# Performance work log

Measured on AMD Instinct MI355X. Metric: run time of the kernel, lower is better.

Reference implementation:

```python
import jax, jax.numpy as jnp
import numpy as np

B, T, H = 64, 1024, 256

def _lstm_cell(x, h, c, Wih, Whh, bih, bhh):
    # torch gate order: i, f, g, o
    gates = x @ Wih.T + h @ Whh.T + bih + bhh  # [B, 4H]
    i, f, g, o = jnp.split(gates, 4, axis=-1)
    i = jax.nn.sigmoid(i)
    f = jax.nn.sigmoid(f)
    g = jnp.tanh(g)
    o = jax.nn.sigmoid(o)
    c_new = f * c + i * g
    h_new = o * jnp.tanh(c_new)
    return h_new, c_new


def setup_inputs() -> dict:
    key = jax.random.key(0)
    ks = jax.random.split(key, 11)
    s = 1.0 / np.sqrt(H)
    def u(k, shape):
        return jax.random.uniform(k, shape, jnp.float32, -s, s)
    return {
        "x": jax.random.normal(ks[0], (B, T, 1), jnp.float32),
        "enc_Wih": u(ks[1], (4 * H, 1)),
        "enc_Whh": u(ks[2], (4 * H, H)),
        "enc_bih": u(ks[3], (4 * H,)),
        "enc_bhh": u(ks[4], (4 * H,)),
        "dec_Wih": u(ks[5], (4 * H, 1)),
        "dec_Whh": u(ks[6], (4 * H, H)),
        "dec_bih": u(ks[7], (4 * H,)),
        "dec_bhh": u(ks[8], (4 * H,)),
        "lin_W": u(ks[9], (1, 2 * H)),
        "lin_b": u(ks[10], (1,)),
    }


def reference(x, enc_Wih, enc_Whh, enc_bih, enc_bhh,
              dec_Wih, dec_Whh, dec_bih, dec_bhh, lin_W, lin_b):
    b = x.shape[0]
    h = x.shape[2] * 0  # placeholder, not used
    hidden = enc_Whh.shape[1]

    x_t = jnp.transpose(x, (1, 0, 2))  # [T, B, 1]

    # ---- encoder: single-layer LSTM over time ----
    def enc_step(carry, xt):
        hh, cc = carry
        hh, cc = _lstm_cell(xt, hh, cc, enc_Wih, enc_Whh, enc_bih, enc_bhh)
        return (hh, cc), hh
    h0 = jnp.zeros((b, hidden), x.dtype)
    (h_last, _), enc_seq = jax.lax.scan(enc_step, (h0, h0), x_t)
    encoder_states = jnp.transpose(enc_seq, (1, 0, 2))  # [B, T, H]

    # ---- decoder: LSTMCell + dot attention + linear, per step ----
    def dec_step(carry, xt):
        hx, cx = carry
        hx, cx = _lstm_cell(xt, hx, cx, dec_Wih, dec_Whh, dec_bih, dec_bhh)
        scores = jnp.einsum('bth,bh->bt', encoder_states, hx)  # dot attention
        attn = jax.nn.softmax(scores, axis=1)
        ctx = jnp.einsum('bt,bth->bh', attn, encoder_states)
        updated = jnp.concatenate([ctx, hx], axis=1)  # [B, 2H]
        res = updated @ lin_W.T + lin_b  # [B, 1]
        return (hx, cx), res

    cx0 = jnp.zeros_like(h_last)
    _, outs = jax.lax.scan(dec_step, (h_last, cx0), x_t)  # [T, B, 1]
    return jnp.transpose(outs, (1, 0, 2))  # [B, T, 1]
```

## Files before the change

### kernel.cpp

```cpp
#include <hip/hip_runtime.h>
#include <math.h>

#define HD 256
#define GD 1024
#define TT 1024
#define BB 64
#define NT 512

__device__ __forceinline__ float sig_(float x)  { return 1.f / (1.f + __expf(-x)); }
__device__ __forceinline__ float tanh_(float x) { return 1.f - 2.f / (1.f + __expf(2.f * x)); }

__global__ __launch_bounds__(256) void prep_kernel(
    const float* __restrict__ eW, const float* __restrict__ eb1, const float* __restrict__ eb2,
    const float* __restrict__ dW, const float* __restrict__ db1, const float* __restrict__ db2,
    float* __restrict__ WTe, float* __restrict__ WTd,
    float* __restrict__ be, float* __restrict__ bd,
    unsigned long long* __restrict__ ex_all)
{
    int idx = blockIdx.x * 256 + threadIdx.x;
    if (idx < GD * HD) {
        int j = idx / HD, k = idx % HD;
        WTe[k * GD + j] = eW[idx];
        WTd[k * GD + j] = dW[idx];
    }
    if (idx < GD) {
        be[idx] = eb1[idx] + eb2[idx];
        bd[idx] = db1[idx] + db2[idx];
    }
    if (idx < 2 * BB * 2 * 256) ex_all[idx] = 0ULL;
}

__global__ __launch_bounds__(NT, 2) void lstm_scan_coop(
    const float* __restrict__ x,
    const float* __restrict__ Wih,
    const float* __restrict__ bias,
    const float* __restrict__ WT,
    const float* __restrict__ h_init,
    float* __restrict__ states,
    unsigned long long* __restrict__ ex)
{
    const int b   = blockIdx.x & 63;
    const int q   = blockIdx.x >> 6;
    const int tid = threadIdx.x;
    const int s   = tid & 3;
    const int jj  = tid >> 2;
    const int gate = jj >> 5;
    const int kk0  = (jj & 31) * 2;
    const int r0   = gate * 64 + kk0;
    const int jg0  = gate * 256 + q * 64 + kk0;

    __shared__ float h_rep[4][264];
    __shared__ float act_s[256];
    __shared__ float x_s[TT];

    float4 w0[16], w1[16];
    {
        const float* basek = WT + (size_t)(s * 64) * GD;
        #pragma unroll
        for (int i = 0; i < 16; ++i) {
            const float* p0 = basek + (size_t)(4 * i) * GD + jg0;
            w0[i] = make_float4(p0[0], p0[GD], p0[2 * GD], p0[3 * GD]);
            const float* p1 = p0 + 1;
            w1[i] = make_float4(p1[0], p1[GD], p1[2 * GD], p1[3 * GD]);
        }
    }
    const float wih0 = Wih[jg0], wih1 = Wih[jg0 + 1];
    const float bj0  = bias[jg0], bj1  = bias[jg0 + 1];

    for (int i = tid; i < TT; i += NT) x_s[i] = x[b * TT + i];
    if (tid < 256) {
        float hv = h_init ? h_init[((size_t)b * TT + (TT - 1)) * HD + tid] : 0.f;
        h_rep[tid >> 6][tid & 63] = hv;
    }
    float c = 0.f;
    __syncthreads();

    for (int t = 0; t < TT; ++t) {
        const float xt = x_s[t];
        float a0p, a1p, a0q = 0.f, a1q = 0.f;
        if (s == 0) { a0p = fmaf(xt, wih0, bj0); a1p = fmaf(xt, wih1, bj1); }
        else        { a0p = 0.f;                 a1p = 0.f; }
        const float4* h4 = (const float4*)(&h_rep[s][0]);
        #pragma unroll
        for (int i = 0; i < 8; ++i) {
            float4 hv = h4[i];
            a0p = fmaf(hv.x, w0[i].x, a0p); a0p = fmaf(hv.y, w0[i].y, a0p);
            a0p = fmaf(hv.z, w0[i].z, a0p); a0p = fmaf(hv.w, w0[i].w, a0p);
            a1p = fmaf(hv.x, w1[i].x, a1p); a1p = fmaf(hv.y, w1[i].y, a1p);
            a1p = fmaf(hv.z, w1[i].z, a1p); a1p = fmaf(hv.w, w1[i].w, a1p);
        }
        #pragma unroll
        for (int i = 8; i < 16; ++i) {
            float4 hv = h4[i];
            a0q = fmaf(hv.x, w0[i].x, a0q); a0q = fmaf(hv.y, w0[i].y, a0q);
            a0q = fmaf(hv.z, w0[i].z, a0q); a0q = fmaf(hv.w, w0[i].w, a0q);
            a1q = fmaf(hv.x, w1[i].x, a1q); a1q = fmaf(hv.y, w1[i].y, a1q);
            a1q = fmaf(hv.z, w1[i].z, a1q); a1q = fmaf(hv.w, w1[i].w, a1q);
        }
        float a0 = a0p + a0q;
        float a1 = a1p + a1q;
        a0 += __shfl_xor(a0, 1); a0 += __shfl_xor(a0, 2);
        a1 += __shfl_xor(a1, 1); a1 += __shfl_xor(a1, 2);
        if (s == 0) {
            float2 av;
            av.x = (gate == 2) ? tanh_(a0) : sig_(a0);
            av.y = (gate == 2) ? tanh_(a1) : sig_(a1);
            *(float2*)(&act_s[r0]) = av;
        }
        __syncthreads();

        unsigned long long* slot = ex + ((size_t)b * 2 + (t & 1)) * 256;
        if (tid < 256) {
            const int dq = tid >> 6, dk = tid & 63;
            if (dq == q) {
                float gi = act_s[dk], gf = act_s[64 + dk], gg = act_s[128 + dk], go = act_s[192 + dk];
                c = fmaf(gf, c, gi * gg);
                float h = go * tanh_(c);
                unsigned long long pk = ((unsigned long long)(unsigned)(t + 1) << 32)
                                      | (unsigned long long)__float_as_uint(h);
                __hip_atomic_store(&slot[tid], pk, __ATOMIC_RELAXED, __HIP_MEMORY_SCOPE_AGENT);
                h_rep[q][dk] = h;
                states[((size_t)(b * TT + t)) * HD + tid] = h;
            } else {
                unsigned long long u;
                do {
                    u = __hip_atomic_load(&slot[tid], __ATOMIC_RELAXED, __HIP_MEMORY_SCOPE_AGENT);
                } while ((unsigned)(u >> 32) != (unsigned)(t + 1));
                h_rep[dq][dk] = __uint_as_float((unsigned)u);
            }
        }
        __syncthreads();
    }
}

__global__ __launch_bounds__(256) void proj_kernel(
    const float* __restrict__ enc_states, const float* __restrict__ dec_hs,
    const float* __restrict__ linW, float* __restrict__ ew, float* __restrict__ hw)
{
    const int lane = threadIdx.x & 63;
    const int wid  = blockIdx.x * 4 + (threadIdx.x >> 6);
    const int nw   = gridDim.x * 4;
    const float4 w1 = ((const float4*)linW)[lane];
    const float4 w2 = ((const float4*)(linW + HD))[lane];
    for (int o = wid; o < BB * TT; o += nw) {
        float4 v1 = ((const float4*)(enc_states + (size_t)o * HD))[lane];
        float4 v2 = ((const float4*)(dec_hs     + (size_t)o * HD))[lane];
        float s1 = v1.x * w1.x + v1.y * w1.y + v1.z * w1.z + v1.w * w1.w;
        float s2 = v2.x * w2.x + v2.y * w2.y + v2.z * w2.z + v2.w * w2.w;
        #pragma unroll
        for (int m = 1; m < 64; m <<= 1) {
            s1 += __shfl_xor(s1, m);
            s2 += __shfl_xor(s2, m);
        }
        if (lane == 0) { ew[o] = s1; hw[o] = s2; }
    }
}

#define TD2  32
#define TEC2 256
#define KC2  32
__global__ __launch_bounds__(256) void attn_kernel(
    const float* __restrict__ enc_states,
    const float* __restrict__ dec_hs,
    const float* __restrict__ ew, const float* __restrict__ hw,
    const float* __restrict__ lin_b,
    float* __restrict__ out)
{
    const int b   = blockIdx.y;
    const int td0 = blockIdx.x * TD2;
    const int tid = threadIdx.x;
    const int tdt = tid >> 5;
    const int tet = tid & 31;

    __shared__ float Hx[HD][TD2 + 4];
    __shared__ float E[KC2][TEC2];

    {
        const int td = tid >> 3;
        const int kc = (tid & 7) * 32;
        const float* src = dec_hs + ((size_t)b * TT + td0 + td) * HD + kc;
        #pragma unroll
        for (int qq = 0; qq < 8; ++qq) {
            float4 v = ((const float4*)(src + qq * 4))[0];
            Hx[kc + qq * 4 + 0][td] = v.x;
            Hx[kc + qq * 4 + 1][td] = v.y;
            Hx[kc + qq * 4 + 2][td] = v.z;
            Hx[kc + qq * 4 + 3][td] = v.w;
        }
    }

    float M[4]  = {-1e30f, -1e30f, -1e30f, -1e30f};
    float Nm[4] = {0.f, 0.f, 0.f, 0.f};
    float Dn[4] = {0.f, 0.f, 0.f, 0.f};

    for (int tc = 0; tc < TT / TEC2; ++tc) {
        const int te0 = tc * TEC2;
        float S[4][8] = {{0.f}};
        for (int kc = 0; kc < HD / KC2; ++kc) {
            const int k0 = kc * KC2;
            __syncthreads();
            {
                const float* src = enc_states + ((size_t)b * TT + te0 + tid) * HD + k0;
                #pragma unroll
                for (int qq = 0; qq < 8; ++qq) {
                    float4 v = ((const float4*)(src + qq * 4))[0];
                    E[qq * 4 + 0][tid] = v.x;
                    E[qq * 4 + 1][tid] = v.y;
                    E[qq * 4 + 2][tid] = v.z;
                    E[qq * 4 + 3][tid] = v.w;
                }
            }
            __syncthreads();
            #pragma unroll 4
            for (int k = 0; k < KC2; ++k) {
                const float4 hx4 = *(const float4*)(&Hx[k0 + k][tdt * 4]);
                #pragma unroll
                for (int i = 0; i < 8; ++i) {
                    const float e = E[k][tet + 32 * i];
                    S[0][i] = fmaf(hx4.x, e, S[0][i]);
                    S[1][i] = fmaf(hx4.y, e, S[1][i]);
                    S[2][i] = fmaf(hx4.z, e, S[2][i]);
                    S[3][i] = fmaf(hx4.w, e, S[3][i]);
                }
            }
        }
        float ewv[8];
        #pragma unroll
        for (int i = 0; i < 8; ++i) ewv[i] = ew[(size_t)b * TT + te0 + tet + 32 * i];
        #pragma unroll
        for (int r = 0; r < 4; ++r) {
            float cm = S[r][0];
            #pragma unroll
            for (int i = 1; i < 8; ++i) cm = fmaxf(cm, S[r][i]);
            #pragma unroll
            for (int m = 1; m < 32; m <<= 1) cm = fmaxf(cm, __shfl_xor(cm, m));
            const float newM  = fmaxf(M[r], cm);
            const float scale = __expf(M[r] - newM);
            float nl = 0.f, dl = 0.f;
            #pragma unroll
            for (int i = 0; i < 8; ++i) {
                const float p = __expf(S[r][i] - newM);
                dl += p;
                nl = fmaf(p, ewv[i], nl);
            }
            #pragma unroll
            for (int m = 1; m < 32; m <<= 1) {
                nl += __shfl_xor(nl, m);
                dl += __shfl_xor(dl, m);
            }
            Nm[r] = Nm[r] * scale + nl;
            Dn[r] = Dn[r] * scale + dl;
            M[r]  = newM;
        }
    }

    if (tet == 0) {
        const float lb = lin_b[0];
        #pragma unroll
        for (int r = 0; r < 4; ++r) {
            const int td = td0 + tdt * 4 + r;
            out[(size_t)b * TT + td] = Nm[r] / Dn[r] + hw[(size_t)b * TT + td] + lb;
        }
    }
}

extern "C" void kernel_launch(void* const* d_in, const int* in_sizes, int n_in,
                              void* d_out, int out_size, void* d_ws, size_t ws_size,
                              hipStream_t stream)
{
    const float* x    = (const float*)d_in[0];
    const float* eWih = (const float*)d_in[1];
    const float* eWhh = (const float*)d_in[2];
    const float* ebih = (const float*)d_in[3];
    const float* ebhh = (const float*)d_in[4];
    const float* dWih = (const float*)d_in[5];
    const float* dWhh = (const float*)d_in[6];
    const float* dbih = (const float*)d_in[7];
    const float* dbhh = (const float*)d_in[8];
    const float* linW = (const float*)d_in[9];
    const float* linb = (const float*)d_in[10];
    float* out = (float*)d_out;

    float* p = (float*)d_ws;
    float* WTe = p;        p += (size_t)GD * HD;
    float* WTd = p;        p += (size_t)GD * HD;
    float* be  = p;        p += GD;
    float* bd  = p;        p += GD;
    float* enc_states = p; p += (size_t)BB * TT * HD;
    float* dec_hs = p;     p += (size_t)BB * TT * HD;
    float* ew = p;         p += (size_t)BB * TT;
    float* hw = p;         p += (size_t)BB * TT;
    unsigned long long* ex_e = (unsigned long long*)p; p += (size_t)BB * 2 * 256 * 2;
    unsigned long long* ex_d = (unsigned long long*)p; p += (size_t)BB * 2 * 256 * 2;

    prep_kernel<<<(GD * HD + 255) / 256, 256, 0, stream>>>(
        eWhh, ebih, ebhh, dWhh, dbih, dbhh, WTe, WTd, be, bd, ex_e);

    {
        const float* hi = nullptr;
        void* args[] = {(void*)&x, (void*)&eWih, (void*)&be, (void*)&WTe,
                        (void*)&hi, (void*)&enc_states, (void*)&ex_e};
        hipLaunchCooperativeKernel((void*)lstm_scan_coop, dim3(256), dim3(NT),
                                   args, 0, stream);
    }
    {
        const float* hi = enc_states;
        void* args[] = {(void*)&x, (void*)&dWih, (void*)&bd, (void*)&WTd,
                        (void*)&hi, (void*)&dec_hs, (void*)&ex_d};
        hipLaunchCooperativeKernel((void*)lstm_scan_coop, dim3(256), dim3(NT),
                                   args, 0, stream);
    }

    proj_kernel<<<256, 256, 0, stream>>>(enc_states, dec_hs, linW, ew, hw);
    attn_kernel<<<dim3(TT / TD2, BB), 256, 0, stream>>>(enc_states, dec_hs, ew, hw, linb, out);
}
```

Measured before the change: 3.864 ms.

## Interleave two batch rows per block to overlap exchange latency with compute

Each block now handles two batch rows and a 32-wide hidden slice across 8 slices, instead of one batch row and a 64-wide slice across 4. While it computes the gate matmul for one row, it spin-waits on the cross-block h exchange for the other row. The point is to hide the global atomic exchange latency that dominates each sequential step. In exchange, each block now syncs with 7 peers instead of 3 and holds half as many weights per thread. The phase ordering is more complex, and the wait-then-publish cycle across 8 blocks risks deadlock if the scheduling assumptions are wrong.

```diff
diff --git a/kernel.cpp b/kernel.cpp
--- a/kernel.cpp
+++ b/kernel.cpp
@@ -30,7 +30,7 @@
     if (idx < 2 * BB * 2 * 256) ex_all[idx] = 0ULL;
 }
 
-__global__ __launch_bounds__(NT, 2) void lstm_scan_coop(
+__global__ __launch_bounds__(NT, 2) void lstm_scan_pair(
     const float* __restrict__ x,
     const float* __restrict__ Wih,
     const float* __restrict__ bias,
@@ -39,95 +39,124 @@
     float* __restrict__ states,
     unsigned long long* __restrict__ ex)
 {
-    const int b   = blockIdx.x & 63;
-    const int q   = blockIdx.x >> 6;
+    const int pair = blockIdx.x & 31;
+    const int sl   = blockIdx.x >> 5;
+    const int b0 = 2 * pair, b1 = 2 * pair + 1;
     const int tid = threadIdx.x;
-    const int s   = tid & 3;
-    const int jj  = tid >> 2;
-    const int gate = jj >> 5;
-    const int kk0  = (jj & 31) * 2;
-    const int r0   = gate * 64 + kk0;
-    const int jg0  = gate * 256 + q * 64 + kk0;
-
-    __shared__ float h_rep[4][264];
-    __shared__ float act_s[256];
-    __shared__ float x_s[TT];
-
-    float4 w0[16], w1[16];
+    const int r    = tid >> 2;
+    const int s    = tid & 3;
+    const int gate = r >> 5;
+    const int dim  = r & 31;
+    const int jg   = gate * 256 + sl * 32 + dim;
+
+    __shared__ float h0s[4][264];
+    __shared__ float h1s[4][264];
+    __shared__ float act0[128];
+    __shared__ float act1[128];
+    __shared__ float x_s[2][TT];
+
+    float4 w[16];
     {
-        const float* basek = WT + (size_t)(s * 64) * GD;
+        const float* bk = WT + (size_t)(s * 64) * GD + jg;
         #pragma unroll
         for (int i = 0; i < 16; ++i) {
-            const float* p0 = basek + (size_t)(4 * i) * GD + jg0;
-            w0[i] = make_float4(p0[0], p0[GD], p0[2 * GD], p0[3 * GD]);
-            const float* p1 = p0 + 1;
-            w1[i] = make_float4(p1[0], p1[GD], p1[2 * GD], p1[3 * GD]);
-        }
-    }
-    const float wih0 = Wih[jg0], wih1 = Wih[jg0 + 1];
-    const float bj0  = bias[jg0], bj1  = bias[jg0 + 1];
-
-    for (int i = tid; i < TT; i += NT) x_s[i] = x[b * TT + i];
+            const float* p0 = bk + (size_t)(4 * i) * GD;
+            w[i] = make_float4(p0[0], p0[GD], p0[2 * GD], p0[3 * GD]);
+        }
+    }
+    const float wih = Wih[jg], bj = bias[jg];
+
+    for (int i = tid; i < TT; i += NT) {
+        x_s[0][i] = x[b0 * TT + i];
+        x_s[1][i] = x[b1 * TT + i];
+    }
     if (tid < 256) {
-        float hv = h_init ? h_init[((size_t)b * TT + (TT - 1)) * HD + tid] : 0.f;
-        h_rep[tid >> 6][tid & 63] = hv;
-    }
-    float c = 0.f;
+        float hv = h_init ? h_init[((size_t)b0 * TT + (TT - 1)) * HD + tid] : 0.f;
+        h0s[tid >> 6][tid & 63] = hv;
+    } else {
+        int gd = tid - 256;
+        float hv = h_init ? h_init[((size_t)b1 * TT + (TT - 1)) * HD + gd] : 0.f;
+        h1s[gd >> 6][gd & 63] = hv;
+    }
+    float c0 = 0.f, c1 = 0.f;
     __syncthreads();
 
+    unsigned long long* ex0 = ex + (size_t)b0 * 2 * 256;
+    unsigned long long* ex1 = ex + (size_t)b1 * 2 * 256;
+
     for (int t = 0; t < TT; ++t) {
-        const float xt = x_s[t];
-        float a0p, a1p, a0q = 0.f, a1q = 0.f;
-        if (s == 0) { a0p = fmaf(xt, wih0, bj0); a1p = fmaf(xt, wih1, bj1); }
-        else        { a0p = 0.f;                 a1p = 0.f; }
-        const float4* h4 = (const float4*)(&h_rep[s][0]);
-        #pragma unroll
-        for (int i = 0; i < 8; ++i) {
-            float4 hv = h4[i];
-            a0p = fmaf(hv.x, w0[i].x, a0p); a0p = fmaf(hv.y, w0[i].y, a0p);
-            a0p = fmaf(hv.z, w0[i].z, a0p); a0p = fmaf(hv.w, w0[i].w, a0p);
-            a1p = fmaf(hv.x, w1[i].x, a1p); a1p = fmaf(hv.y, w1[i].y, a1p);
-            a1p = fmaf(hv.z, w1[i].z, a1p); a1p = fmaf(hv.w, w1[i].w, a1p);
-        }
-        #pragma unroll
-        for (int i = 8; i < 16; ++i) {
-            float4 hv = h4[i];
-            a0q = fmaf(hv.x, w0[i].x, a0q); a0q = fmaf(hv.y, w0[i].y, a0q);
-            a0q = fmaf(hv.z, w0[i].z, a0q); a0q = fmaf(hv.w, w0[i].w, a0q);
-            a1q = fmaf(hv.x, w1[i].x, a1q); a1q = fmaf(hv.y, w1[i].y, a1q);
-            a1q = fmaf(hv.z, w1[i].z, a1q); a1q = fmaf(hv.w, w1[i].w, a1q);
-        }
-        float a0 = a0p + a0q;
-        float a1 = a1p + a1q;
-        a0 += __shfl_xor(a0, 1); a0 += __shfl_xor(a0, 2);
-        a1 += __shfl_xor(a1, 1); a1 += __shfl_xor(a1, 2);
-        if (s == 0) {
-            float2 av;
-            av.x = (gate == 2) ? tanh_(a0) : sig_(a0);
-            av.y = (gate == 2) ? tanh_(a1) : sig_(a1);
-            *(float2*)(&act_s[r0]) = av;
+        {
+            const float xt = x_s[0][t];
+            float a = (s == 0) ? fmaf(xt, wih, bj) : 0.f;
+            const float4* h4 = (const float4*)&h0s[s][0];
+            #pragma unroll
+            for (int i = 0; i < 16; ++i) {
+                float4 hv = h4[i];
+                a = fmaf(hv.x, w[i].x, a); a = fmaf(hv.y, w[i].y, a);
+                a = fmaf(hv.z, w[i].z, a); a = fmaf(hv.w, w[i].w, a);
+            }
+            a += __shfl_xor(a, 1); a += __shfl_xor(a, 2);
+            if (s == 0) act0[r] = (gate == 2) ? tanh_(a) : sig_(a);
+        }
+        if (t > 0 && tid >= 288) {
+            const int u  = tid - 288;
+            const int gd = u + (u >= sl * 32 ? 32 : 0);
+            unsigned long long* slot = ex1 + (size_t)(t & 1) * 256 + gd;
+            unsigned long long v;
+            do { v = __hip_atomic_load(slot, __ATOMIC_RELAXED, __HIP_MEMORY_SCOPE_AGENT); }
+            while ((unsigned)(v >> 32) != (unsigned)t);
+            h1s[gd >> 6][gd & 63] = __uint_as_float((unsigned)v);
         }
         __syncthreads();
 
-        unsigned long long* slot = ex + ((size_t)b * 2 + (t & 1)) * 256;
-        if (tid < 256) {
-            const int dq = tid >> 6, dk = tid & 63;
-            if (dq == q) {
-                float gi = act_s[dk], gf = act_s[64 + dk], gg = act_s[128 + dk], go = act_s[192 + dk];
-                c = fmaf(gf, c, gi * gg);
-                float h = go * tanh_(c);
-                unsigned long long pk = ((unsigned long long)(unsigned)(t + 1) << 32)
-                                      | (unsigned long long)__float_as_uint(h);
-                __hip_atomic_store(&slot[tid], pk, __ATOMIC_RELAXED, __HIP_MEMORY_SCOPE_AGENT);
-                h_rep[q][dk] = h;
-                states[((size_t)(b * TT + t)) * HD + tid] = h;
-            } else {
-                unsigned long long u;
-                do {
-                    u = __hip_atomic_load(&slot[tid], __ATOMIC_RELAXED, __HIP_MEMORY_SCOPE_AGENT);
-                } while ((unsigned)(u >> 32) != (unsigned)(t + 1));
-                h_rep[dq][dk] = __uint_as_float((unsigned)u);
-            }
+        if (tid < 32) {
+            float gi = act0[tid], gf = act0[32 + tid], gg = act0[64 + tid], go = act0[96 + tid];
+            c0 = fmaf(gf, c0, gi * gg);
+            float h = go * tanh_(c0);
+            const int gd = sl * 32 + tid;
+            unsigned long long pk = ((unsigned long long)(unsigned)(t + 1) << 32)
+                                  | (unsigned long long)__float_as_uint(h);
+            __hip_atomic_store(ex0 + (size_t)((t + 1) & 1) * 256 + gd, pk,
+                               __ATOMIC_RELAXED, __HIP_MEMORY_SCOPE_AGENT);
+            h0s[gd >> 6][gd & 63] = h;
+            states[((size_t)(b0 * TT + t)) * HD + gd] = h;
+        }
+        {
+            const float xt = x_s[1][t];
+            float a = (s == 0) ? fmaf(xt, wih, bj) : 0.f;
+            const float4* h4 = (const float4*)&h1s[s][0];
+            #pragma unroll
+            for (int i = 0; i < 16; ++i) {
+                float4 hv = h4[i];
+                a = fmaf(hv.x, w[i].x, a); a = fmaf(hv.y, w[i].y, a);
+                a = fmaf(hv.z, w[i].z, a); a = fmaf(hv.w, w[i].w, a);
+            }
+            a += __shfl_xor(a, 1); a += __shfl_xor(a, 2);
+            if (s == 0) act1[r] = (gate == 2) ? tanh_(a) : sig_(a);
+        }
+        __syncthreads();
+
+        if (tid >= 256 && tid < 288) {
+            const int l = tid - 256;
+            float gi = act1[l], gf = act1[32 + l], gg = act1[64 + l], go = act1[96 + l];
+            c1 = fmaf(gf, c1, gi * gg);
+            float h = go * tanh_(c1);
+            const int gd = sl * 32 + l;
+            unsigned long long pk = ((unsigned long long)(unsigned)(t + 1) << 32)
+                                  | (unsigned long long)__float_as_uint(h);
+            __hip_atomic_store(ex1 + (size_t)((t + 1) & 1) * 256 + gd, pk,
+                               __ATOMIC_RELAXED, __HIP_MEMORY_SCOPE_AGENT);
+            h1s[gd >> 6][gd & 63] = h;
+            states[((size_t)(b1 * TT + t)) * HD + gd] = h;
+        }
+        if (tid >= 32 && tid < 256 && t < TT - 1) {
+            const int u  = tid - 32;
+            const int gd = u + (u >= sl * 32 ? 32 : 0);
+            unsigned long long* slot = ex0 + (size_t)((t + 1) & 1) * 256 + gd;
+            unsigned long long v;
+            do { v = __hip_atomic_load(slot, __ATOMIC_RELAXED, __HIP_MEMORY_SCOPE_AGENT); }
+            while ((unsigned)(v >> 32) != (unsigned)(t + 1));
+            h0s[gd >> 6][gd & 63] = __uint_as_float((unsigned)v);
         }
         __syncthreads();
     }
@@ -300,14 +329,14 @@
         const float* hi = nullptr;
         void* args[] = {(void*)&x, (void*)&eWih, (void*)&be, (void*)&WTe,
                         (void*)&hi, (void*)&enc_states, (void*)&ex_e};
-        hipLaunchCooperativeKernel((void*)lstm_scan_coop, dim3(256), dim3(NT),
+        hipLaunchCooperativeKernel((void*)lstm_scan_pair, dim3(256), dim3(NT),
                                    args, 0, stream);
     }
     {
         const float* hi = enc_states;
         void* args[] = {(void*)&x, (void*)&dWih, (void*)&bd, (void*)&WTd,
                         (void*)&hi, (void*)&dec_hs, (void*)&ex_d};
-        hipLaunchCooperativeKernel((void*)lstm_scan_coop, dim3(256), dim3(NT),
+        hipLaunchCooperativeKernel((void*)lstm_scan_pair, dim3(256), dim3(NT),
                                    args, 0, stream);
     }
 
```

Result: slower. 4.484 ms (+16.0%).

## Run each batch's LSTM scan in one workgroup with fp16 register-resident weights

Applied to the files above, without the earlier changes.

Replaces the cooperative four-block-per-batch LSTM scan with a single 512-thread workgroup per batch element. Cross-block atomic handshakes are replaced by __syncthreads. Recurrent weights are converted to fp16 and consumed with packed fdot2. Most of the weight matrix (176 of 256 columns) stays in registers, and the remainder streams from a global interleaved layout each step. This removes inter-block spin-wait latency per timestep but cuts parallelism to 64 workgroups, adds per-step global weight reads, and lowers the precision of weights and hidden state to fp16.

```diff
diff --git a/kernel.cpp b/kernel.cpp
--- a/kernel.cpp
+++ b/kernel.cpp
@@ -5,7 +5,13 @@
 #define GD 1024
 #define TT 1024
 #define BB 64
-#define NT 512
+#define KV 176
+#define KS 80
+#define NSC (KS / 8)
+
+typedef _Float16 half2v __attribute__((ext_vector_type(2)));
+
+struct h4c { half2v a, b, c, d; };
 
 __device__ __forceinline__ float sig_(float x)  { return 1.f / (1.f + __expf(-x)); }
 __device__ __forceinline__ float tanh_(float x) { return 1.f - 2.f / (1.f + __expf(2.f * x)); }
@@ -13,121 +19,113 @@
 __global__ __launch_bounds__(256) void prep_kernel(
     const float* __restrict__ eW, const float* __restrict__ eb1, const float* __restrict__ eb2,
     const float* __restrict__ dW, const float* __restrict__ db1, const float* __restrict__ db2,
-    float* __restrict__ WTe, float* __restrict__ WTd,
-    float* __restrict__ be, float* __restrict__ bd,
-    unsigned long long* __restrict__ ex_all)
+    _Float16* __restrict__ Wv_e, _Float16* __restrict__ Ws_e,
+    _Float16* __restrict__ Wv_d, _Float16* __restrict__ Ws_d,
+    float* __restrict__ be, float* __restrict__ bd)
 {
     int idx = blockIdx.x * 256 + threadIdx.x;
     if (idx < GD * HD) {
         int j = idx / HD, k = idx % HD;
-        WTe[k * GD + j] = eW[idx];
-        WTd[k * GD + j] = dW[idx];
+        float we = eW[idx], wd = dW[idx];
+        if (k < KV) {
+            Wv_e[(size_t)j * KV + k] = (_Float16)we;
+            Wv_d[(size_t)j * KV + k] = (_Float16)wd;
+        } else {
+            int cc = (k - KV) >> 3, i = (k - KV) & 7;
+            Ws_e[((size_t)cc * GD + j) * 8 + i] = (_Float16)we;
+            Ws_d[((size_t)cc * GD + j) * 8 + i] = (_Float16)wd;
+        }
     }
     if (idx < GD) {
         be[idx] = eb1[idx] + eb2[idx];
         bd[idx] = db1[idx] + db2[idx];
     }
-    if (idx < 2 * BB * 2 * 256) ex_all[idx] = 0ULL;
-}
-
-__global__ __launch_bounds__(NT, 2) void lstm_scan_coop(
+}
+
+__global__ __launch_bounds__(512, 1) void lstm_scan_cu(
     const float* __restrict__ x,
     const float* __restrict__ Wih,
     const float* __restrict__ bias,
-    const float* __restrict__ WT,
+    const _Float16* __restrict__ Wv,
+    const _Float16* __restrict__ Wstr,
     const float* __restrict__ h_init,
-    float* __restrict__ states,
-    unsigned long long* __restrict__ ex)
-{
-    const int b   = blockIdx.x & 63;
-    const int q   = blockIdx.x >> 6;
-    const int tid = threadIdx.x;
-    const int s   = tid & 3;
-    const int jj  = tid >> 2;
-    const int gate = jj >> 5;
-    const int kk0  = (jj & 31) * 2;
-    const int r0   = gate * 64 + kk0;
-    const int jg0  = gate * 256 + q * 64 + kk0;
-
-    __shared__ float h_rep[4][264];
-    __shared__ float act_s[256];
+    float* __restrict__ states)
+{
+    const int b  = blockIdx.x;
+    const int t0 = threadIdx.x;
+    const int jA = t0, jB = t0 + 512;
+
     __shared__ float x_s[TT];
-
-    float4 w0[16], w1[16];
+    __shared__ float act_s[GD];
+    __shared__ __align__(16) _Float16 h16[HD];
+
+    half2v wA[KV / 2], wB[KV / 2];
     {
-        const float* basek = WT + (size_t)(s * 64) * GD;
-        #pragma unroll
-        for (int i = 0; i < 16; ++i) {
-            const float* p0 = basek + (size_t)(4 * i) * GD + jg0;
-            w0[i] = make_float4(p0[0], p0[GD], p0[2 * GD], p0[3 * GD]);
-            const float* p1 = p0 + 1;
-            w1[i] = make_float4(p1[0], p1[GD], p1[2 * GD], p1[3 * GD]);
-        }
-    }
-    const float wih0 = Wih[jg0], wih1 = Wih[jg0 + 1];
-    const float bj0  = bias[jg0], bj1  = bias[jg0 + 1];
-
-    for (int i = tid; i < TT; i += NT) x_s[i] = x[b * TT + i];
-    if (tid < 256) {
-        float hv = h_init ? h_init[((size_t)b * TT + (TT - 1)) * HD + tid] : 0.f;
-        h_rep[tid >> 6][tid & 63] = hv;
+        const half2v* pa = (const half2v*)(Wv + (size_t)jA * KV);
+        const half2v* pb = (const half2v*)(Wv + (size_t)jB * KV);
+        #pragma unroll
+        for (int i = 0; i < KV / 2; ++i) { wA[i] = pa[i]; wB[i] = pb[i]; }
+    }
+    const float wihA = Wih[jA], wihB = Wih[jB];
+    const float bjA  = bias[jA], bjB  = bias[jB];
+
+    for (int i = t0; i < TT; i += 512) x_s[i] = x[b * TT + i];
+    if (t0 < HD) {
+        float hv = h_init ? h_init[((size_t)b * TT + (TT - 1)) * HD + t0] : 0.f;
+        h16[t0] = (_Float16)hv;
     }
     float c = 0.f;
     __syncthreads();
 
     for (int t = 0; t < TT; ++t) {
         const float xt = x_s[t];
-        float a0p, a1p, a0q = 0.f, a1q = 0.f;
-        if (s == 0) { a0p = fmaf(xt, wih0, bj0); a1p = fmaf(xt, wih1, bj1); }
-        else        { a0p = 0.f;                 a1p = 0.f; }
-        const float4* h4 = (const float4*)(&h_rep[s][0]);
-        #pragma unroll
-        for (int i = 0; i < 8; ++i) {
-            float4 hv = h4[i];
-            a0p = fmaf(hv.x, w0[i].x, a0p); a0p = fmaf(hv.y, w0[i].y, a0p);
-            a0p = fmaf(hv.z, w0[i].z, a0p); a0p = fmaf(hv.w, w0[i].w, a0p);
-            a1p = fmaf(hv.x, w1[i].x, a1p); a1p = fmaf(hv.y, w1[i].y, a1p);
-            a1p = fmaf(hv.z, w1[i].z, a1p); a1p = fmaf(hv.w, w1[i].w, a1p);
-        }
-        #pragma unroll
-        for (int i = 8; i < 16; ++i) {
-            float4 hv = h4[i];
-            a0q = fmaf(hv.x, w0[i].x, a0q); a0q = fmaf(hv.y, w0[i].y, a0q);
-            a0q = fmaf(hv.z, w0[i].z, a0q); a0q = fmaf(hv.w, w0[i].w, a0q);
-            a1q = fmaf(hv.x, w1[i].x, a1q); a1q = fmaf(hv.y, w1[i].y, a1q);
-            a1q = fmaf(hv.z, w1[i].z, a1q); a1q = fmaf(hv.w, w1[i].w, a1q);
-        }
-        float a0 = a0p + a0q;
-        float a1 = a1p + a1q;
-        a0 += __shfl_xor(a0, 1); a0 += __shfl_xor(a0, 2);
-        a1 += __shfl_xor(a1, 1); a1 += __shfl_xor(a1, 2);
-        if (s == 0) {
-            float2 av;
-            av.x = (gate == 2) ? tanh_(a0) : sig_(a0);
-            av.y = (gate == 2) ? tanh_(a1) : sig_(a1);
-            *(float2*)(&act_s[r0]) = av;
-        }
+        float aA = fmaf(xt, wihA, bjA);
+        float aB = fmaf(xt, wihB, bjB);
+
+        const h4c* h8 = (const h4c*)h16;
+
+        #pragma unroll
+        for (int cch = 0; cch < KV / 8; ++cch) {
+            h4c hv = h8[cch];
+            aA = __builtin_amdgcn_fdot2(wA[cch * 4 + 0], hv.a, aA, false);
+            aA = __builtin_amdgcn_fdot2(wA[cch * 4 + 1], hv.b, aA, false);
+            aA = __builtin_amdgcn_fdot2(wA[cch * 4 + 2], hv.c, aA, false);
+            aA = __builtin_amdgcn_fdot2(wA[cch * 4 + 3], hv.d, aA, false);
+            aB = __builtin_amdgcn_fdot2(wB[cch * 4 + 0], hv.a, aB, false);
+            aB = __builtin_amdgcn_fdot2(wB[cch * 4 + 1], hv.b, aB, false);
+            aB = __builtin_amdgcn_fdot2(wB[cch * 4 + 2], hv.c, aB, false);
+            aB = __builtin_amdgcn_fdot2(wB[cch * 4 + 3], hv.d, aB, false);
+        }
+
+        const _Float16* ws = Wstr;
+        asm volatile("" : "+v"(ws));
+        const h4c* sA = (const h4c*)(ws + (size_t)jA * 8);
+        const h4c* sB = (const h4c*)(ws + (size_t)jB * 8);
+        #pragma unroll
+        for (int cc = 0; cc < NSC; ++cc) {
+            h4c wa = sA[(size_t)cc * GD];
+            h4c wb = sB[(size_t)cc * GD];
+            h4c hv = h8[KV / 8 + cc];
+            aA = __builtin_amdgcn_fdot2(wa.a, hv.a, aA, false);
+            aA = __builtin_amdgcn_fdot2(wa.b, hv.b, aA, false);
+            aA = __builtin_amdgcn_fdot2(wa.c, hv.c, aA, false);
+            aA = __builtin_amdgcn_fdot2(wa.d, hv.d, aA, false);
+            aB = __builtin_amdgcn_fdot2(wb.a, hv.a, aB, false);
+            aB = __builtin_amdgcn_fdot2(wb.b, hv.b, aB, false);
+            aB = __builtin_amdgcn_fdot2(wb.c, hv.c, aB, false);
+            aB = __builtin_amdgcn_fdot2(wb.d, hv.d, aB, false);
+        }
+
+        act_s[jA] = sig_(aA);
+        act_s[jB] = (t0 < 256) ? tanh_(aB) : sig_(aB);
         __syncthreads();
 
-        unsigned long long* slot = ex + ((size_t)b * 2 + (t & 1)) * 256;
-        if (tid < 256) {
-            const int dq = tid >> 6, dk = tid & 63;
-            if (dq == q) {
-                float gi = act_s[dk], gf = act_s[64 + dk], gg = act_s[128 + dk], go = act_s[192 + dk];
-                c = fmaf(gf, c, gi * gg);
-                float h = go * tanh_(c);
-                unsigned long long pk = ((unsigned long long)(unsigned)(t + 1) << 32)
-                                      | (unsigned long long)__float_as_uint(h);
-                __hip_atomic_store(&slot[tid], pk, __ATOMIC_RELAXED, __HIP_MEMORY_SCOPE_AGENT);
-                h_rep[q][dk] = h;
-                states[((size_t)(b * TT + t)) * HD + tid] = h;
-            } else {
-                unsigned long long u;
-                do {
-                    u = __hip_atomic_load(&slot[tid], __ATOMIC_RELAXED, __HIP_MEMORY_SCOPE_AGENT);
-                } while ((unsigned)(u >> 32) != (unsigned)(t + 1));
-                h_rep[dq][dk] = __uint_as_float((unsigned)u);
-            }
+        if (t0 < HD) {
+            float gi = act_s[t0], gf = act_s[256 + t0], gg = act_s[512 + t0], go = act_s[768 + t0];
+            c = fmaf(gf, c, gi * gg);
+            float h = go * tanh_(c);
+            states[((size_t)(b * TT + t)) * HD + t0] = h;
+            h16[t0] = (_Float16)h;
         }
         __syncthreads();
     }
@@ -282,34 +280,22 @@
     float* out = (float*)d_out;
 
     float* p = (float*)d_ws;
-    float* WTe = p;        p += (size_t)GD * HD;
-    float* WTd = p;        p += (size_t)GD * HD;
     float* be  = p;        p += GD;
     float* bd  = p;        p += GD;
     float* enc_states = p; p += (size_t)BB * TT * HD;
     float* dec_hs = p;     p += (size_t)BB * TT * HD;
     float* ew = p;         p += (size_t)BB * TT;
     float* hw = p;         p += (size_t)BB * TT;
-    unsigned long long* ex_e = (unsigned long long*)p; p += (size_t)BB * 2 * 256 * 2;
-    unsigned long long* ex_d = (unsigned long long*)p; p += (size_t)BB * 2 * 256 * 2;
+    _Float16* Wv_e = (_Float16*)p;
+    _Float16* Ws_e = Wv_e + (size_t)GD * KV;
+    _Float16* Wv_d = Ws_e + (size_t)NSC * GD * 8;
+    _Float16* Ws_d = Wv_d + (size_t)GD * KV;
 
     prep_kernel<<<(GD * HD + 255) / 256, 256, 0, stream>>>(
-        eWhh, ebih, ebhh, dWhh, dbih, dbhh, WTe, WTd, be, bd, ex_e);
-
-    {
-        const float* hi = nullptr;
-        void* args[] = {(void*)&x, (void*)&eWih, (void*)&be, (void*)&WTe,
-                        (void*)&hi, (void*)&enc_states, (void*)&ex_e};
-        hipLaunchCooperativeKernel((void*)lstm_scan_coop, dim3(256), dim3(NT),
-                                   args, 0, stream);
-    }
-    {
-        const float* hi = enc_states;
-        void* args[] = {(void*)&x, (void*)&dWih, (void*)&bd, (void*)&WTd,
-                        (void*)&hi, (void*)&dec_hs, (void*)&ex_d};
-        hipLaunchCooperativeKernel((void*)lstm_scan_coop, dim3(256), dim3(NT),
-                                   args, 0, stream);
-    }
+        eWhh, ebih, ebhh, dWhh, dbih, dbhh, Wv_e, Ws_e, Wv_d, Ws_d, be, bd);
+
+    lstm_scan_cu<<<BB, 512, 0, stream>>>(x, eWih, be, Wv_e, Ws_e, nullptr, enc_states);
+    lstm_scan_cu<<<BB, 512, 0, stream>>>(x, dWih, bd, Wv_d, Ws_d, enc_states, dec_hs);
 
     proj_kernel<<<256, 256, 0, stream>>>(enc_states, dec_hs, linW, ew, hw);
     attn_kernel<<<dim3(TT / TD2, BB), 256, 0, stream>>>(enc_states, dec_hs, ew, hw, linb, out);
```

Measured after the change: 5.255 ms. +36.0%, slower.
